# Kernel optimization log

Measured on AMD Instinct MI355X. Metric: run time of the kernel, lower is better.

## Reference

```python
import jax, jax.numpy as jnp
import numpy as np

T, B, F, U, CODES = 256, 128, 1024, 512, 1024


def setup_inputs() -> dict:
    key = jax.random.key(0)
    ks = jax.random.split(key, 6)
    s_in = 1.0 / np.sqrt(F)
    s_rec = 1.0 / np.sqrt(U)
    return {
        "x": jax.random.normal(ks[0], (T, B, F), dtype=jnp.float32),
        "mask": jax.random.uniform(ks[1], (T, B), dtype=jnp.float32),
        "W_in": jax.random.normal(ks[2], (F, 4 * U), dtype=jnp.float32) * s_in,
        "W_rec": jax.random.normal(ks[3], (U, 4 * U), dtype=jnp.float32) * s_rec,
        "b_lstm": jnp.zeros((4 * U,), dtype=jnp.float32),
        "W_dense": jax.random.normal(ks[4], (U, CODES), dtype=jnp.float32) * s_rec,
        "b_dense": jnp.zeros((CODES,), dtype=jnp.float32),
    }


def _lstm_seq(x, W_in, W_rec, b_lstm):
    # x: [T, B, F] time-major; Keras gate order: i, f, g(candidate), o
    Bn = x.shape[1]
    u = W_rec.shape[0]
    # Precompute input projections for all timesteps: [T, B, 4U]
    xz = jnp.einsum('tbf,fg->tbg', x, W_in) + b_lstm

    def step(carry, xz_t):
        h, c = carry
        z = xz_t + h @ W_rec  # [B, 4U]
        i, f, g, o = jnp.split(z, 4, axis=-1)
        i = jax.nn.sigmoid(i)
        f = jax.nn.sigmoid(f)
        g = jnp.tanh(g)
        o = jax.nn.sigmoid(o)
        c = f * c + i * g
        h = o * jnp.tanh(c)
        return (h, c), h

    h0 = jnp.zeros((Bn, u), dtype=x.dtype)
    c0 = jnp.zeros((Bn, u), dtype=x.dtype)
    _, h_seq = jax.lax.scan(step, (h0, c0), xz)
    return h_seq  # [T, B, U]


def reference(x, mask, W_in, W_rec, b_lstm, W_dense, b_dense):
    # Original: input [T,B,F] -> transpose to [B,T,F] -> LSTM -> transpose back.
    # Equivalent: scan directly over the leading time axis.
    h_seq = _lstm_seq(x, W_in, W_rec, b_lstm)          # [T, B, U]
    masked = h_seq * mask[..., None]                    # [T, B, U]
    logits = jax.nn.relu(masked @ W_dense + b_dense)    # [T, B, CODES]
    return jax.nn.softmax(logits, axis=-1)
```

## Files before the change

### kernel.cpp

```cpp
#include <hip/hip_runtime.h>

typedef unsigned short u16;
typedef unsigned int   u32;
typedef unsigned long long u64;
using f32x4  = __attribute__((ext_vector_type(4))) float;
using bf16x8 = __attribute__((ext_vector_type(8))) short;
using u32x4  = __attribute__((ext_vector_type(4))) u32;
using u32x2  = __attribute__((ext_vector_type(2))) u32;


__device__ __forceinline__ u16 f2bf(float f) {
    union { float f; u32 u; } v; v.f = f;
    u32 r = v.u + 0x7fffu + ((v.u >> 16) & 1u);
    return (u16)(r >> 16);
}
__device__ __forceinline__ float bf2f(u16 h) {
    union { u32 u; float f; } v; v.u = ((u32)h) << 16; return v.f;
}
__device__ __forceinline__ float sigmoid_f(float x) { return 1.f / (1.f + __expf(-x)); }
__device__ __forceinline__ float tanh_f(float x) {
    x = fminf(fmaxf(x, -15.f), 15.f);
    float e = __expf(2.f * x);
    return (e - 1.f) / (e + 1.f);
}

__global__ __launch_bounds__(256) void convx_k(const float* __restrict__ in,
                                               u16* __restrict__ out) {
    size_t i = (size_t)blockIdx.x * 256 + threadIdx.x;
    float4 v = ((const float4*)in)[i];
    u32 lo = (u32)f2bf(v.x) | ((u32)f2bf(v.y) << 16);
    u32 hi = (u32)f2bf(v.z) | ((u32)f2bf(v.w) << 16);
    u32x2 o; o.x = lo; o.y = hi;
    ((u32x2*)out)[i] = o;
}

__global__ __launch_bounds__(256) void convT_k(const float* __restrict__ in,
                                               u16* __restrict__ out, int K, int N) {
    __shared__ float tile[32][33];
    int kt = blockIdx.y * 32, nt = blockIdx.x * 32;
    int c = threadIdx.x & 31, r4 = threadIdx.x >> 5;
#pragma unroll
    for (int rr = 0; rr < 4; ++rr) {
        int r = rr * 8 + r4;
        tile[r][c] = in[(size_t)(kt + r) * N + nt + c];
    }
    __syncthreads();
#pragma unroll
    for (int rr = 0; rr < 4; ++rr) {
        int r = rr * 8 + r4;
        out[(size_t)(nt + r) * K + kt + c] = f2bf(tile[c][r]);
    }
}

template <int K, int MODE>
__global__ __launch_bounds__(256) void gemm_bt(const u16* __restrict__ A,
                                               const u16* __restrict__ Bt,
                                               const float* __restrict__ bias,
                                               void* __restrict__ Cout, int N) {
    __shared__ u16 Al[128][40];
    __shared__ u16 Bl[128][40];
    const int m0 = blockIdx.x * 128, n0 = blockIdx.y * 128;
    const int tid = threadIdx.x, lane = tid & 63, wave = tid >> 6;
    const int wm = (wave >> 1) * 64, wn = (wave & 1) * 64;
    f32x4 acc[4][4] = {};
    const int srow  = tid >> 1;
    const int skoff = (tid & 1) * 16;
    const u16* ag = A  + (size_t)(m0 + srow) * K + skoff;
    const u16* bg = Bt + (size_t)(n0 + srow) * K + skoff;

    for (int k0 = 0; k0 < K; k0 += 32) {
        u32x4 av0 = *(const u32x4*)(ag + k0);
        u32x4 av1 = *(const u32x4*)(ag + k0 + 8);
        u32x4 bv0 = *(const u32x4*)(bg + k0);
        u32x4 bv1 = *(const u32x4*)(bg + k0 + 8);
        __syncthreads();
        *(u32x4*)&Al[srow][skoff]     = av0;
        *(u32x4*)&Al[srow][skoff + 8] = av1;
        *(u32x4*)&Bl[srow][skoff]     = bv0;
        *(u32x4*)&Bl[srow][skoff + 8] = bv1;
        __syncthreads();
        bf16x8 af[4], bf[4];
#pragma unroll
        for (int i = 0; i < 4; ++i)
            af[i] = *(const bf16x8*)&Al[wm + i * 16 + (lane & 15)][(lane >> 4) * 8];
#pragma unroll
        for (int i = 0; i < 4; ++i)
            bf[i] = *(const bf16x8*)&Bl[wn + i * 16 + (lane & 15)][(lane >> 4) * 8];
#pragma unroll
        for (int mi = 0; mi < 4; ++mi)
#pragma unroll
            for (int ni = 0; ni < 4; ++ni)
                acc[mi][ni] = __builtin_amdgcn_mfma_f32_16x16x32_bf16(
                    af[mi], bf[ni], acc[mi][ni], 0, 0, 0);
    }
#pragma unroll
    for (int mi = 0; mi < 4; ++mi)
#pragma unroll
        for (int ni = 0; ni < 4; ++ni) {
            int col = n0 + wn + ni * 16 + (lane & 15);
            float bv = bias[col];
            int rbase = m0 + wm + mi * 16 + (lane >> 4) * 4;
#pragma unroll
            for (int r = 0; r < 4; ++r) {
                float v = acc[mi][ni][r] + bv;
                size_t off = (size_t)(rbase + r) * N + col;
                if (MODE == 1) ((float*)Cout)[off] = fmaxf(v, 0.f);
                else           ((u16*)Cout)[off]   = f2bf(v);
            }
        }
}

__global__ __launch_bounds__(256, 1) void lstm_kernel(const u16* __restrict__ xz,
                                                      const float* __restrict__ mask,
                                                      const float* __restrict__ W_rec,
                                                      u32* __restrict__ flags,
                                                      u16* __restrict__ hbuf,
                                                      u16* __restrict__ h_seq) {
    __shared__ __align__(16) u16   hsf[8192];
    __shared__ __align__(16) float zxs[1024];
    __shared__ __align__(16) float msk[4096];
    char* hsf_b = (char*)hsf;
    const int tid = threadIdx.x, lane = tid & 63, wave = tid >> 6;
    const int gb = blockIdx.x & 7, gu = blockIdx.x >> 3;
    const int b0 = gb << 4, u0 = gu << 4;
    u32* flg = flags + (gb << 5);

    bf16x8 wreg[16];
#pragma unroll
    for (int c = 0; c < 4; ++c) {
#pragma unroll
        for (int q = 0; q < 8; ++q) {
            int idx = q * 256 + tid;
            int kk = idx >> 4, s16 = idx & 15;
            const float4 w4 = *(const float4*)(W_rec + (size_t)(c * 128 + kk) * 2048 +
                                               (s16 >> 2) * 512 + u0 + (s16 & 3) * 4);
            u64 pk = (u64)f2bf(w4.x) | ((u64)f2bf(w4.y) << 16) |
                     ((u64)f2bf(w4.z) << 32) | ((u64)f2bf(w4.w) << 48);
            ((u64*)hsf)[kk * 16 + s16] = pk;
        }
        __syncthreads();
#pragma unroll
        for (int wl = 0; wl < 4; ++wl) {
            union { bf16x8 v; u16 s[8]; } wb;
#pragma unroll
            for (int e = 0; e < 8; ++e)
                wb.s[e] = hsf[(wl * 32 + (lane >> 4) * 8 + e) * 64 + wave * 16 + (lane & 15)];
            wreg[c * 4 + wl] = wb.v;
        }
        __syncthreads();
    }
#pragma unroll
    for (int k = 0; k < 16; ++k) {
        int idx = k * 256 + tid;
        msk[idx] = mask[(idx >> 4) * 128 + b0 + (idx & 15)];
    }
    const int bl = tid >> 4, ul = tid & 15;
    float creg = 0.f;
    __syncthreads();

    u16 xzr0, xzr1, xzr2, xzr3;
    u16 xzn0, xzn1, xzn2, xzn3;
    {
        const u16* xzp = xz + (((size_t)(b0 + bl)) << 11) + u0 + ul;
        xzr0 = xzp[0]; xzr1 = xzp[512]; xzr2 = xzp[1024]; xzr3 = xzp[1536];
    }

    for (int t = 0; t < 256; ++t) {
        if (t) {
            if (lane < 32) {
                u32 v;
                do {
                    v = __hip_atomic_load(&flg[lane], __ATOMIC_RELAXED,
                                          __HIP_MEMORY_SCOPE_SYSTEM);
                } while (v < (u32)t);
            }
            asm volatile("" ::: "memory");
        }
        {
            const u16* hb = hbuf + ((size_t)(t & 1) << 16);
            u64 sv[8];
#pragma unroll
            for (int i2 = 0; i2 < 4; ++i2) {
                int r = (tid >> 6) * 4 + i2;
                const u64* p = (const u64*)(hb + ((size_t)(b0 + r) << 9)) + 2 * (tid & 63);
                sv[2 * i2]     = __hip_atomic_load(p,     __ATOMIC_RELAXED,
                                                   __HIP_MEMORY_SCOPE_SYSTEM);
                sv[2 * i2 + 1] = __hip_atomic_load(p + 1, __ATOMIC_RELAXED,
                                                   __HIP_MEMORY_SCOPE_SYSTEM);
            }
            {
                size_t tn = (t < 255) ? (size_t)(t + 1) : 255;
                const u16* xzp = xz + ((tn * 128 + b0 + bl) << 11) + u0 + ul;
                xzn0 = xzp[0]; xzn1 = xzp[512]; xzn2 = xzp[1024]; xzn3 = xzp[1536];
            }
#pragma unroll
            for (int i2 = 0; i2 < 4; ++i2) {
                int r = (tid >> 6) * 4 + i2, s = tid & 63;
                int w32 = s >> 2, g = s & 3, l2 = (g << 4) | r;
                u32x4 val;
                val.x = (u32)sv[2 * i2];     val.y = (u32)(sv[2 * i2] >> 32);
                val.z = (u32)sv[2 * i2 + 1]; val.w = (u32)(sv[2 * i2 + 1] >> 32);
                *(u32x4*)(hsf_b + w32 * 1024 + ((l2 * 16) ^ ((w32 & 7) << 4))) = val;
            }
        }
        __syncthreads();
        {
            f32x4 acc0 = {0.f, 0.f, 0.f, 0.f}, acc1 = {0.f, 0.f, 0.f, 0.f};
#pragma unroll
            for (int i = 0; i < 8; ++i) {
                const int wa = 2 * i, wb2 = 2 * i + 1;
                bf16x8 a0 = *(const bf16x8*)(hsf_b + wa * 1024 +
                                             ((lane * 16) ^ ((wa & 7) << 4)));
                bf16x8 a1 = *(const bf16x8*)(hsf_b + wb2 * 1024 +
                                             ((lane * 16) ^ ((wb2 & 7) << 4)));
                acc0 = __builtin_amdgcn_mfma_f32_16x16x32_bf16(a0, wreg[wa],  acc0, 0, 0, 0);
                acc1 = __builtin_amdgcn_mfma_f32_16x16x32_bf16(a1, wreg[wb2], acc1, 0, 0, 0);
            }
            acc0 += acc1;
#pragma unroll
            for (int r = 0; r < 4; ++r)
                zxs[wave * 256 + (((lane >> 4) << 2) + r) * 16 + (lane & 15)] = acc0[r];
        }
        __syncthreads();
        {
            float zi = zxs[tid]       + bf2f(xzr0);
            float zf = zxs[256 + tid] + bf2f(xzr1);
            float zg = zxs[512 + tid] + bf2f(xzr2);
            float zo = zxs[768 + tid] + bf2f(xzr3);
            float ig = sigmoid_f(zi), fg = sigmoid_f(zf);
            float gg = tanh_f(zg),    og = sigmoid_f(zo);
            creg = fg * creg + ig * gg;
            float h = og * tanh_f(creg);
            u32 hu = (u32)f2bf(h);
            u32 nb = (u32)__shfl_xor((int)hu, 1);
            if (!(ul & 1)) {
                u32 pair = (hu & 0xFFFFu) | (nb << 16);
                u16* hbn = hbuf + ((size_t)((t + 1) & 1) << 16);
                __hip_atomic_store((u32*)hbn + ((((size_t)(b0 + bl) << 9) + u0 + ul) >> 1),
                                   pair, __ATOMIC_RELAXED, __HIP_MEMORY_SCOPE_SYSTEM);
            }
            float hm = h * msk[t * 16 + bl];
            h_seq[(((size_t)t * 128 + b0 + bl) << 9) + u0 + ul] = f2bf(hm);
            xzr0 = xzn0; xzr1 = xzn1; xzr2 = xzn2; xzr3 = xzn3;
        }
        __syncthreads();
        if (tid == 0 && t != 255)
            __hip_atomic_store(&flg[gu], (u32)(t + 1), __ATOMIC_RELAXED,
                               __HIP_MEMORY_SCOPE_SYSTEM);
    }
}

__global__ __launch_bounds__(256) void softmax_k(float* __restrict__ io) {
    __shared__ float red[4];
    float4* p = (float4*)(io + (size_t)blockIdx.x * 1024);
    const int tid = threadIdx.x, lane = tid & 63, wave = tid >> 6;
    float4 v = p[tid];
    float m = fmaxf(fmaxf(v.x, v.y), fmaxf(v.z, v.w));
#pragma unroll
    for (int off = 32; off; off >>= 1) m = fmaxf(m, __shfl_xor(m, off));
    if (lane == 0) red[wave] = m;
    __syncthreads();
    m = fmaxf(fmaxf(red[0], red[1]), fmaxf(red[2], red[3]));
    float4 e;
    e.x = __expf(v.x - m); e.y = __expf(v.y - m);
    e.z = __expf(v.z - m); e.w = __expf(v.w - m);
    float s = e.x + e.y + e.z + e.w;
#pragma unroll
    for (int off = 32; off; off >>= 1) s += __shfl_xor(s, off);
    __syncthreads();
    if (lane == 0) red[wave] = s;
    __syncthreads();
    s = red[0] + red[1] + red[2] + red[3];
    float inv = 1.f / s;
    v.x = e.x * inv; v.y = e.y * inv; v.z = e.z * inv; v.w = e.w * inv;
    p[tid] = v;
}

extern "C" void kernel_launch(void* const* d_in, const int* in_sizes, int n_in,
                              void* d_out, int out_size, void* d_ws, size_t ws_size,
                              hipStream_t stream) {
    const float* x       = (const float*)d_in[0];
    const float* mask    = (const float*)d_in[1];
    const float* W_in    = (const float*)d_in[2];
    const float* W_rec   = (const float*)d_in[3];
    const float* b_lstm  = (const float*)d_in[4];
    const float* W_dense = (const float*)d_in[5];
    const float* b_dense = (const float*)d_in[6];

    char* ws = (char*)d_ws;
    u16* W_inT = (u16*)(ws);
    u16* W_dT  = (u16*)(ws + (4ull << 20));
    u32* flags = (u32*)(ws + (5ull << 20));
    u16* hbuf  = (u16*)(ws + (5ull << 20) + 1024);
    u16* x_bf  = (u16*)(ws + (8ull << 20));
    u16* h_seq = (u16*)(ws + (8ull << 20));
    if (ws_size < 75497472ull) return;

    convx_k<<<32768, 256, 0, stream>>>(x, x_bf);
    convT_k<<<dim3(64, 32), 256, 0, stream>>>(W_in, W_inT, 1024, 2048);
    convT_k<<<dim3(32, 16), 256, 0, stream>>>(W_dense, W_dT, 512, 1024);
    hipMemsetAsync(flags, 0, 1024 + 131072, stream);

    gemm_bt<1024, 0><<<dim3(256, 16), 256, 0, stream>>>(x_bf, W_inT, b_lstm, d_out, 2048);

    {
        const u16* xzp = (const u16*)d_out;
        void* args[] = { (void*)&xzp, (void*)&mask, (void*)&W_rec,
                         (void*)&flags, (void*)&hbuf, (void*)&h_seq };
        hipLaunchCooperativeKernel((void*)lstm_kernel, dim3(256), dim3(256),
                                   args, 0, stream);
    }

    gemm_bt<512, 1><<<dim3(256, 8), 256, 0, stream>>>(h_seq, W_dT, b_dense, d_out, 1024);
    softmax_k<<<32768, 256, 0, stream>>>((float*)d_out);
}
```

Baseline: 966.6 us.

## Fuse x bf16 conversion into input GEMM and use per-wave LSTM step flags

```diff
diff --git a/kernel.cpp b/kernel.cpp
--- a/kernel.cpp
+++ b/kernel.cpp
@@ -22,16 +22,6 @@
     x = fminf(fmaxf(x, -15.f), 15.f);
     float e = __expf(2.f * x);
     return (e - 1.f) / (e + 1.f);
-}
-
-__global__ __launch_bounds__(256) void convx_k(const float* __restrict__ in,
-                                               u16* __restrict__ out) {
-    size_t i = (size_t)blockIdx.x * 256 + threadIdx.x;
-    float4 v = ((const float4*)in)[i];
-    u32 lo = (u32)f2bf(v.x) | ((u32)f2bf(v.y) << 16);
-    u32 hi = (u32)f2bf(v.z) | ((u32)f2bf(v.w) << 16);
-    u32x2 o; o.x = lo; o.y = hi;
-    ((u32x2*)out)[i] = o;
 }
 
 __global__ __launch_bounds__(256) void convT_k(const float* __restrict__ in,
@@ -110,6 +100,73 @@
         }
 }
 
+__global__ __launch_bounds__(256) void gemm_af32(const float* __restrict__ A,
+                                                 const u16* __restrict__ Bt,
+                                                 const float* __restrict__ bias,
+                                                 u16* __restrict__ Cout) {
+    const int K = 1024, N = 2048;
+    __shared__ u16 Al[128][40];
+    __shared__ u16 Bl[128][40];
+    const int m0 = blockIdx.x * 128, n0 = blockIdx.y * 128;
+    const int tid = threadIdx.x, lane = tid & 63, wave = tid >> 6;
+    const int wm = (wave >> 1) * 64, wn = (wave & 1) * 64;
+    f32x4 acc[4][4] = {};
+    const int srow  = tid >> 1;
+    const int skoff = (tid & 1) * 16;
+    const float* ag = A  + (size_t)(m0 + srow) * K + skoff;
+    const u16*   bg = Bt + (size_t)(n0 + srow) * K + skoff;
+
+    for (int k0 = 0; k0 < K; k0 += 32) {
+        float4 a0 = *(const float4*)(ag + k0);
+        float4 a1 = *(const float4*)(ag + k0 + 4);
+        float4 a2 = *(const float4*)(ag + k0 + 8);
+        float4 a3 = *(const float4*)(ag + k0 + 12);
+        u32x4 bv0 = *(const u32x4*)(bg + k0);
+        u32x4 bv1 = *(const u32x4*)(bg + k0 + 8);
+        u32x4 pa0, pa1;
+        pa0.x = (u32)f2bf(a0.x) | ((u32)f2bf(a0.y) << 16);
+        pa0.y = (u32)f2bf(a0.z) | ((u32)f2bf(a0.w) << 16);
+        pa0.z = (u32)f2bf(a1.x) | ((u32)f2bf(a1.y) << 16);
+        pa0.w = (u32)f2bf(a1.z) | ((u32)f2bf(a1.w) << 16);
+        pa1.x = (u32)f2bf(a2.x) | ((u32)f2bf(a2.y) << 16);
+        pa1.y = (u32)f2bf(a2.z) | ((u32)f2bf(a2.w) << 16);
+        pa1.z = (u32)f2bf(a3.x) | ((u32)f2bf(a3.y) << 16);
+        pa1.w = (u32)f2bf(a3.z) | ((u32)f2bf(a3.w) << 16);
+        __syncthreads();
+        *(u32x4*)&Al[srow][skoff]     = pa0;
+        *(u32x4*)&Al[srow][skoff + 8] = pa1;
+        *(u32x4*)&Bl[srow][skoff]     = bv0;
+        *(u32x4*)&Bl[srow][skoff + 8] = bv1;
+        __syncthreads();
+        bf16x8 af[4], bf[4];
+#pragma unroll
+        for (int i = 0; i < 4; ++i)
+            af[i] = *(const bf16x8*)&Al[wm + i * 16 + (lane & 15)][(lane >> 4) * 8];
+#pragma unroll
+        for (int i = 0; i < 4; ++i)
+            bf[i] = *(const bf16x8*)&Bl[wn + i * 16 + (lane & 15)][(lane >> 4) * 8];
+#pragma unroll
+        for (int mi = 0; mi < 4; ++mi)
+#pragma unroll
+            for (int ni = 0; ni < 4; ++ni)
+                acc[mi][ni] = __builtin_amdgcn_mfma_f32_16x16x32_bf16(
+                    af[mi], bf[ni], acc[mi][ni], 0, 0, 0);
+    }
+#pragma unroll
+    for (int mi = 0; mi < 4; ++mi)
+#pragma unroll
+        for (int ni = 0; ni < 4; ++ni) {
+            int col = n0 + wn + ni * 16 + (lane & 15);
+            float bv = bias[col];
+            int rbase = m0 + wm + mi * 16 + (lane >> 4) * 4;
+#pragma unroll
+            for (int r = 0; r < 4; ++r) {
+                float v = acc[mi][ni][r] + bv;
+                Cout[(size_t)(rbase + r) * N + col] = f2bf(v);
+            }
+        }
+}
+
 __global__ __launch_bounds__(256, 1) void lstm_kernel(const u16* __restrict__ xz,
                                                       const float* __restrict__ mask,
                                                       const float* __restrict__ W_rec,
@@ -123,7 +180,7 @@
     const int tid = threadIdx.x, lane = tid & 63, wave = tid >> 6;
     const int gb = blockIdx.x & 7, gu = blockIdx.x >> 3;
     const int b0 = gb << 4, u0 = gu << 4;
-    u32* flg = flags + (gb << 5);
+    u32* flg = flags + (gb << 7);
 
     bf16x8 wreg[16];
 #pragma unroll
@@ -158,25 +215,27 @@
     float creg = 0.f;
     __syncthreads();
 
-    u16 xzr0, xzr1, xzr2, xzr3;
-    u16 xzn0, xzn1, xzn2, xzn3;
-    {
-        const u16* xzp = xz + (((size_t)(b0 + bl)) << 11) + u0 + ul;
-        xzr0 = xzp[0]; xzr1 = xzp[512]; xzr2 = xzp[1024]; xzr3 = xzp[1536];
-    }
+    const u16* xzbase = xz + (((size_t)(b0 + bl)) << 11) + u0 + ul;
+    u16 xzr0 = xzbase[0], xzr1 = xzbase[512], xzr2 = xzbase[1024], xzr3 = xzbase[1536];
+    u16 xzn0 = xzr0, xzn1 = xzr1, xzn2 = xzr2, xzn3 = xzr3;
+    const u16* xznext = xzbase + (1 << 18);
+    u16* hseqp = h_seq + (((size_t)(b0 + bl)) << 9) + u0 + ul;
 
     for (int t = 0; t < 256; ++t) {
         if (t) {
-            if (lane < 32) {
-                u32 v;
-                do {
-                    v = __hip_atomic_load(&flg[lane], __ATOMIC_RELAXED,
-                                          __HIP_MEMORY_SCOPE_SYSTEM);
-                } while (v < (u32)t);
-            }
+            const u64* fp = (const u64*)flg + lane;
+            u64 v;
+            do {
+                v = __hip_atomic_load(fp, __ATOMIC_RELAXED, __HIP_MEMORY_SCOPE_SYSTEM);
+            } while ((u32)v < (u32)t || (u32)(v >> 32) < (u32)t);
             asm volatile("" ::: "memory");
         }
         {
+            if (t < 255) {
+                xzn0 = xznext[0]; xzn1 = xznext[512];
+                xzn2 = xznext[1024]; xzn3 = xznext[1536];
+                xznext += (1 << 18);
+            }
             const u16* hb = hbuf + ((size_t)(t & 1) << 16);
             u64 sv[8];
 #pragma unroll
@@ -187,11 +246,6 @@
                                                    __HIP_MEMORY_SCOPE_SYSTEM);
                 sv[2 * i2 + 1] = __hip_atomic_load(p + 1, __ATOMIC_RELAXED,
                                                    __HIP_MEMORY_SCOPE_SYSTEM);
-            }
-            {
-                size_t tn = (t < 255) ? (size_t)(t + 1) : 255;
-                const u16* xzp = xz + ((tn * 128 + b0 + bl) << 11) + u0 + ul;
-                xzn0 = xzp[0]; xzn1 = xzp[512]; xzn2 = xzp[1024]; xzn3 = xzp[1536];
             }
 #pragma unroll
             for (int i2 = 0; i2 < 4; ++i2) {
@@ -236,17 +290,20 @@
             if (!(ul & 1)) {
                 u32 pair = (hu & 0xFFFFu) | (nb << 16);
                 u16* hbn = hbuf + ((size_t)((t + 1) & 1) << 16);
-                __hip_atomic_store((u32*)hbn + ((((size_t)(b0 + bl) << 9) + u0 + ul) >> 1),
-                                   pair, __ATOMIC_RELAXED, __HIP_MEMORY_SCOPE_SYSTEM);
+                u32* hp = (u32*)hbn + ((((size_t)(b0 + bl) << 9) + u0 + ul) >> 1);
+                __hip_atomic_store(hp, pair, __ATOMIC_RELAXED, __HIP_MEMORY_SCOPE_SYSTEM);
             }
             float hm = h * msk[t * 16 + bl];
-            h_seq[(((size_t)t * 128 + b0 + bl) << 9) + u0 + ul] = f2bf(hm);
+            *hseqp = f2bf(hm);
+            hseqp += (1 << 16);
             xzr0 = xzn0; xzr1 = xzn1; xzr2 = xzn2; xzr3 = xzn3;
         }
-        __syncthreads();
-        if (tid == 0 && t != 255)
-            __hip_atomic_store(&flg[gu], (u32)(t + 1), __ATOMIC_RELAXED,
-                               __HIP_MEMORY_SCOPE_SYSTEM);
+        if (t != 255) {
+            asm volatile("s_waitcnt vmcnt(0)" ::: "memory");
+            if (lane == 0)
+                __hip_atomic_store(&flg[(gu << 2) | wave], (u32)(t + 1),
+                                   __ATOMIC_RELAXED, __HIP_MEMORY_SCOPE_SYSTEM);
+        }
     }
 }
 
@@ -291,17 +348,15 @@
     u16* W_inT = (u16*)(ws);
     u16* W_dT  = (u16*)(ws + (4ull << 20));
     u32* flags = (u32*)(ws + (5ull << 20));
-    u16* hbuf  = (u16*)(ws + (5ull << 20) + 1024);
-    u16* x_bf  = (u16*)(ws + (8ull << 20));
+    u16* hbuf  = (u16*)(ws + (5ull << 20) + 4096);
     u16* h_seq = (u16*)(ws + (8ull << 20));
     if (ws_size < 75497472ull) return;
 
-    convx_k<<<32768, 256, 0, stream>>>(x, x_bf);
     convT_k<<<dim3(64, 32), 256, 0, stream>>>(W_in, W_inT, 1024, 2048);
     convT_k<<<dim3(32, 16), 256, 0, stream>>>(W_dense, W_dT, 512, 1024);
-    hipMemsetAsync(flags, 0, 1024 + 131072, stream);
-
-    gemm_bt<1024, 0><<<dim3(256, 16), 256, 0, stream>>>(x_bf, W_inT, b_lstm, d_out, 2048);
+    hipMemsetAsync(flags, 0, 4096 + 131072, stream);
+
+    gemm_af32<<<dim3(256, 16), 256, 0, stream>>>(x, W_inT, b_lstm, (u16*)d_out);
 
     {
         const u16* xzp = (const u16*)d_out;
```

Result: slower. 1.672 ms (+73.0%).
